# Kernel tuning notes

Measured on AMD Instinct MI355X. Metric: run time of the kernel, lower is better.

## Reference

```python
import jax, jax.numpy as jnp
import numpy as np

ROTARY_DIM = 128
ROTARY_BASE = 10000.0
ATTN_SCALE = 11.313708498984761  # sqrt(d_head=128)
N_HEADS = 16
N_KV = 4


def _apply_rotary(x, rotary_dim, rotary_base):
    # x: [seq, heads, d_head]
    seq_len = x.shape[0]
    dim_pairs = rotary_dim // 2
    freqs = 1.0 / rotary_base ** (jnp.arange(dim_pairs, dtype=jnp.float32) / dim_pairs)
    angles = jnp.outer(jnp.arange(seq_len), freqs)  # [seq, pairs]
    cos = jnp.cos(angles)[:, None, :]
    sin = jnp.sin(angles)[:, None, :]
    x_rot = x[..., :rotary_dim]
    x_pass = x[..., rotary_dim:]
    x1 = x_rot[..., ::2]
    x2 = x_rot[..., 1::2]
    out1 = x1 * cos - x2 * sin
    out2 = x1 * sin + x2 * cos
    rotated = jnp.stack([out1, out2], axis=-1).reshape(x_rot.shape)
    return jnp.concatenate([rotated, x_pass], axis=-1)


def setup_inputs() -> dict:
    key = jax.random.key(0)
    ks = jax.random.split(key, 5)
    seq, d_model, d_head = 4096, 2048, 128
    scale = 1.0 / np.sqrt(d_model)
    return {
        "x": jax.random.normal(ks[0], (seq, d_model), jnp.float32),
        "W_Q": jax.random.normal(ks[1], (N_HEADS, d_model, d_head), jnp.float32) * scale,
        "W_K": jax.random.normal(ks[2], (N_KV, d_model, d_head), jnp.float32) * scale,
        "W_V": jax.random.normal(ks[3], (N_KV, d_model, d_head), jnp.float32) * scale,
        "W_O": jax.random.normal(ks[4], (N_HEADS, d_head, d_model), jnp.float32) * scale,
        "b_Q": jnp.zeros((N_HEADS, d_head), jnp.float32),
        "b_K": jnp.zeros((N_KV, d_head), jnp.float32),
        "b_V": jnp.zeros((N_KV, d_head), jnp.float32),
        "b_O": jnp.zeros((2048,), jnp.float32),
    }


def reference(x, W_Q, W_K, W_V, W_O, b_Q, b_K, b_V, b_O):
    seq_len = x.shape[0]
    q = jnp.einsum('sm,nmh->snh', x, W_Q) + b_Q  # [s, 16, 128]
    k = jnp.einsum('sm,nmh->snh', x, W_K) + b_K  # [s, 4, 128]
    v = jnp.einsum('sm,nmh->snh', x, W_V) + b_V
    q = _apply_rotary(q, ROTARY_DIM, ROTARY_BASE)
    k = _apply_rotary(k, ROTARY_DIM, ROTARY_BASE)
    repeats = N_HEADS // N_KV
    k = jnp.repeat(k, repeats, axis=1)
    v = jnp.repeat(v, repeats, axis=1)
    attn_scores = jnp.einsum('qnh,knh->nqk', q, k) / ATTN_SCALE
    mask = jnp.tril(jnp.ones((seq_len, seq_len), dtype=jnp.bool_))
    attn_scores = jnp.where(mask[None, :, :], attn_scores,
                            jnp.finfo(attn_scores.dtype).min)
    pattern = jax.nn.softmax(attn_scores, axis=-1)
    z = jnp.einsum('nqk,knh->qnh', pattern, v)
    return jnp.einsum('snh,nhm->sm', z, W_O) + b_O
```

## Files before the change

### kernel.cpp

```cpp
#include <hip/hip_runtime.h>
#include <hip/hip_bf16.h>
#include <cstdint>
#include <cstddef>

#define SEQ    4096
#define DM     2048
#define DH     128
#define NH     16
#define NKV    4
#define NC     3072
#define KOFF   2048
#define VOFF   2560
#define Q_SCALE 0.12751730f

using bf16 = __hip_bfloat16;
typedef __bf16 bf16x8 __attribute__((ext_vector_type(8)));
typedef float f32x4 __attribute__((ext_vector_type(4)));
typedef float f32x16 __attribute__((ext_vector_type(16)));

static __device__ inline float bf2f(bf16 x) { return __bfloat162float(x); }
static __device__ inline bf16 f2bf(float x) { return __float2bfloat16(x); }

static __device__ inline void load_lds16(const bf16* g, bf16* l) {
    __builtin_amdgcn_global_load_lds(
        (const __attribute__((address_space(1))) uint32_t*)g,
        (__attribute__((address_space(3))) uint32_t*)l, 16, 0, 0);
}

__global__ void xconv(const float* __restrict__ in, bf16* __restrict__ out) {
    int i = blockIdx.x * 256 + threadIdx.x;
    float4 v = ((const float4*)in)[i];
    bf16 a = f2bf(v.x), b = f2bf(v.y), c = f2bf(v.z), d = f2bf(v.w);
    ushort4 u;
    u.x = *(unsigned short*)&a; u.y = *(unsigned short*)&b;
    u.z = *(unsigned short*)&c; u.w = *(unsigned short*)&d;
    ((ushort4*)out)[i] = u;
}

__global__ void prep_wqkv(const float* __restrict__ WQ, const float* __restrict__ WK,
                          const float* __restrict__ WV, bf16* __restrict__ wt) {
    __shared__ float tl[64][65];
    const int t = threadIdx.x;
    const int m0 = (int)blockIdx.x * 64;
    const int head = (int)blockIdx.y >> 1;
    const int h0 = ((int)blockIdx.y & 1) * 64;
    const float* src = (head < 16) ? WQ + (size_t)head * DM * DH
                     : (head < 20) ? WK + (size_t)(head - 16) * DM * DH
                                   : WV + (size_t)(head - 20) * DM * DH;
    {
        const int r = t >> 2, c = (t & 3) * 16;
        const float* p = src + (size_t)(m0 + r) * DH + h0 + c;
        #pragma unroll
        for (int kk = 0; kk < 4; ++kk) {
            float4 v = *(const float4*)(p + kk * 4);
            tl[r][c + kk * 4 + 0] = v.x; tl[r][c + kk * 4 + 1] = v.y;
            tl[r][c + kk * 4 + 2] = v.z; tl[r][c + kk * 4 + 3] = v.w;
        }
    }
    __syncthreads();
    {
        const int hh = t >> 2, ms = (t & 3) * 16;
        const int j = head * 128 + h0 + hh;
        bf16 tmp[16];
        #pragma unroll
        for (int i = 0; i < 16; ++i) tmp[i] = f2bf(tl[ms + i][hh]);
        bf16* q = wt + (size_t)j * DM + m0 + ms;
        *(bf16x8*)q       = *(bf16x8*)&tmp[0];
        *(bf16x8*)(q + 8) = *(bf16x8*)&tmp[8];
    }
}

__global__ void prep_wo(const float* __restrict__ WO, bf16* __restrict__ wt) {
    __shared__ float tl[64][65];
    const int t = threadIdx.x;
    const int m0 = (int)blockIdx.x * 64;
    const int j0 = (int)blockIdx.y * 64;
    {
        const int r = t >> 2, c = (t & 3) * 16;
        const float* p = WO + (size_t)(m0 + r) * DM + j0 + c;
        #pragma unroll
        for (int kk = 0; kk < 4; ++kk) {
            float4 v = *(const float4*)(p + kk * 4);
            tl[r][c + kk * 4 + 0] = v.x; tl[r][c + kk * 4 + 1] = v.y;
            tl[r][c + kk * 4 + 2] = v.z; tl[r][c + kk * 4 + 3] = v.w;
        }
    }
    __syncthreads();
    {
        const int hh = t >> 2, ms = (t & 3) * 16;
        bf16 tmp[16];
        #pragma unroll
        for (int i = 0; i < 16; ++i) tmp[i] = f2bf(tl[ms + i][hh]);
        bf16* q = wt + (size_t)(j0 + hh) * DM + m0 + ms;
        *(bf16x8*)q       = *(bf16x8*)&tmp[0];
        *(bf16x8*)(q + 8) = *(bf16x8*)&tmp[8];
    }
}

__global__ void prep_bias(const float* __restrict__ bQ, const float* __restrict__ bK,
                          const float* __restrict__ bV, float* __restrict__ bias) {
    int j = blockIdx.x * 256 + threadIdx.x;
    if (j >= NC) return;
    bias[j] = (j < KOFF) ? bQ[j] : (j < VOFF ? bK[j - KOFF] : bV[j - VOFF]);
}

#define BM 128
#define BN 128
#define BK 64

template <typename OutT>
__global__ __launch_bounds__(256)
void gemm_bt(const bf16* __restrict__ A, const bf16* __restrict__ Bt,
             const float* __restrict__ bias, OutT* __restrict__ C, int N) {
    __shared__ __align__(16) bf16 As[BM * BK];
    __shared__ __align__(16) bf16 Bs[BN * BK];
    const int tid = threadIdx.x;
    const int wave = tid >> 6, lane = tid & 63;
    const int quad = lane >> 4, l15 = lane & 15;
    const int wm = (wave >> 1) * 64, wn = (wave & 1) * 64;
    const int m0 = blockIdx.y * BM, n0 = blockIdx.x * BN;

    f32x4 acc[4][4] = {};

    const bf16* gsrc = (wave < 2)
        ? A  + (size_t)(m0 + (wave & 1) * 64) * DM
        : Bt + (size_t)(n0 + (wave & 1) * 64) * DM;
    bf16* lbase = (wave < 2 ? As : Bs) + (wave & 1) * 64 * BK;
    const int lrow = lane >> 3;
    const int gslot = (lane & 7) ^ lrow;
    const bf16* gp = gsrc + (size_t)lrow * DM + gslot * 8;

    const int rsw = l15 & 7;

    for (int k0 = 0; k0 < DM; k0 += BK) {
        __syncthreads();
        #pragma unroll
        for (int cc = 0; cc < 8; ++cc)
            load_lds16(gp + (size_t)cc * 8 * DM + k0, lbase + cc * 8 * BK);
        __syncthreads();

        #pragma unroll
        for (int ks = 0; ks < 2; ++ks) {
            bf16x8 af[4], bfr[4];
            #pragma unroll
            for (int i = 0; i < 4; ++i)
                af[i] = *(const bf16x8*)&As[(wm + i * 16 + l15) * BK + (((ks * 4 + quad) ^ rsw) * 8)];
            #pragma unroll
            for (int j = 0; j < 4; ++j)
                bfr[j] = *(const bf16x8*)&Bs[(wn + j * 16 + l15) * BK + (((ks * 4 + quad) ^ rsw) * 8)];
            #pragma unroll
            for (int i = 0; i < 4; ++i)
                #pragma unroll
                for (int j = 0; j < 4; ++j)
                    acc[i][j] = __builtin_amdgcn_mfma_f32_16x16x32_bf16(af[i], bfr[j], acc[i][j], 0, 0, 0);
        }
    }

    #pragma unroll
    for (int i = 0; i < 4; ++i) {
        int row = m0 + wm + i * 16 + quad * 4;
        #pragma unroll
        for (int j = 0; j < 4; ++j) {
            int col = n0 + wn + j * 16 + l15;
            float bv = bias[col];
            #pragma unroll
            for (int r = 0; r < 4; ++r) {
                float val = acc[i][j][r] + bv;
                if constexpr (sizeof(OutT) == 2)
                    C[(size_t)(row + r) * N + col] = f2bf(val);
                else
                    C[(size_t)(row + r) * N + col] = val;
            }
        }
    }
}

__global__ void sctab(float2* __restrict__ tab) {
    int idx = blockIdx.x * 256 + threadIdx.x;
    int s = idx >> 6, i = idx & 63;
    float inv_freq = __expf(-(float)i * 0.14391156831212788f);
    float ang = (float)s * inv_freq;
    float2 cs;
    cs.x = cosf(ang);
    cs.y = sinf(ang);
    tab[idx] = cs;
}

__global__ void rotary(bf16* __restrict__ qkv, const float2* __restrict__ tab) {
    int idx = blockIdx.x * 256 + threadIdx.x;
    const int QP = SEQ * (NH * DH / 2);
    int s, col, i; float scale;
    if (idx < QP) {
        s = idx >> 10; int p = idx & 1023;
        col = ((p >> 6) * DH) + 2 * (p & 63);
        i = p & 63;
        scale = Q_SCALE;
    } else {
        idx -= QP;
        if (idx >= SEQ * (NKV * DH / 2)) return;
        s = idx >> 8; int p = idx & 255;
        col = KOFF + ((p >> 6) * DH) + 2 * (p & 63);
        i = p & 63;
        scale = 1.0f;
    }
    float2 cs = tab[(s << 6) + i];
    float c = cs.x, sn = cs.y;
    uint32_t u = *(const uint32_t*)(qkv + (size_t)s * NC + col);
    float x1 = __uint_as_float((u & 0xffffu) << 16);
    float x2 = __uint_as_float(u & 0xffff0000u);
    float o1 = (x1 * c - x2 * sn) * scale;
    float o2 = (x1 * sn + x2 * c) * scale;
    bf16 h1 = f2bf(o1), h2 = f2bf(o2);
    uint32_t out = ((uint32_t)(*(unsigned short*)&h2) << 16) | (uint32_t)(*(unsigned short*)&h1);
    *(uint32_t*)(qkv + (size_t)s * NC + col) = out;
}

__global__ void vtrans(const bf16* __restrict__ qkv, bf16* __restrict__ vt) {
    __shared__ bf16 tl[64][72];
    const int t = threadIdx.x;
    const int s0 = (int)(blockIdx.x >> 3) * 64;
    const int c0 = (int)(blockIdx.x & 7) * 64;
    {
        int r = t >> 2, cc = (t & 3) * 16;
        const bf16* p = qkv + (size_t)(s0 + r) * NC + VOFF + c0 + cc;
        *(bf16x8*)&tl[r][cc]     = *(const bf16x8*)p;
        *(bf16x8*)&tl[r][cc + 8] = *(const bf16x8*)(p + 8);
    }
    __syncthreads();
    {
        int dd = t >> 2, sc = (t & 3) * 16;
        int col = c0 + dd;
        bf16 tmp[16];
        #pragma unroll
        for (int j = 0; j < 16; ++j) tmp[j] = tl[sc + j][dd];
        bf16* q = vt + (size_t)col * SEQ + s0 + sc;
        *(bf16x8*)q       = *(bf16x8*)&tmp[0];
        *(bf16x8*)(q + 8) = *(bf16x8*)&tmp[8];
    }
}

__global__ __launch_bounds__(256, 3)
void flash(const bf16* __restrict__ qkv, const bf16* __restrict__ vt,
           bf16* __restrict__ z) {
    __shared__ char smem[33280];
    bf16*  Ks  = (bf16*)smem;
    bf16*  Vs  = (bf16*)(smem + 16384);
    float* lml = (float*)(smem + 32768);
    float* ob  = (float*)smem;

    const int tid = threadIdx.x;
    const int wave = tid >> 6, lane = tid & 63;
    const int l31 = lane & 31, lh = lane >> 5;
    const int ch = wave >> 1;
    const int kh = wave & 1;
    const int bx = blockIdx.x;
    const int qt = 127 - (bx >> 3);
    const int g = (bx >> 1) & 3;
    const int hp = bx & 1;
    const int r_base = qt * 32 + ch * 16;
    const int ktmax = qt >> 1;
    const int rsw = l31 & 7;

    const bf16* kp[4];
    const bf16* vp[4];
    #pragma unroll
    for (int i = 0; i < 4; ++i) {
        const int q = wave * 4 + i;
        const int krow = q * 4 + (lane >> 4);
        kp[i] = qkv + KOFF + g * DH + (size_t)krow * NC + (((lane & 15) ^ (krow & 7)) * 8);
        const int vdd = q * 8 + (lane >> 3);
        vp[i] = vt + (size_t)(g * DH + vdd) * SEQ + (((lane & 7) ^ (vdd & 7)) * 8);
    }

    bf16x8 qf[8];
    {
        const int qrow = r_base + (l31 & 15);
        const int head = g * 4 + hp * 2 + (l31 >> 4);
        const bf16* qp = qkv + (size_t)qrow * NC + head * DH + lh * 8;
        #pragma unroll
        for (int s = 0; s < 8; ++s)
            qf[s] = *(const bf16x8*)(qp + s * 16);
    }

    f32x16 o_acc[4] = {};
    float lsum = 0.0f;

    for (int kt = 0; kt <= ktmax; ++kt) {
        __syncthreads();
        #pragma unroll
        for (int i = 0; i < 4; ++i)
            load_lds16(kp[i], Ks + (wave * 4 + i) * 512);
        #pragma unroll
        for (int i = 0; i < 4; ++i)
            load_lds16(vp[i], Vs + (wave * 4 + i) * 512);
        __syncthreads();
        #pragma unroll
        for (int i = 0; i < 4; ++i) { kp[i] += (size_t)64 * NC; vp[i] += 64; }

        const int key_min = kt * 64 + kh * 32;
        if (key_min <= r_base + 15) {
            f32x16 sacc = {};
            __builtin_amdgcn_s_setprio(1);
            #pragma unroll
            for (int s = 0; s < 8; ++s) {
                bf16x8 kb = *(const bf16x8*)&Ks[(kh * 32 + l31) * 128 + (((lh + 2 * s) ^ rsw) * 8)];
                sacc = __builtin_amdgcn_mfma_f32_32x32x16_bf16(kb, qf[s], sacc, 0, 0, 0);
            }
            __builtin_amdgcn_s_setprio(0);

            const bool needmask = (key_min + 31 > r_base);
            const int qrow = r_base + (l31 & 15);
            float e[16];
            if (needmask) {
                #pragma unroll
                for (int rg = 0; rg < 16; ++rg) {
                    const int keyg = key_min + (rg & 3) + 8 * (rg >> 2) + 4 * lh;
                    float sv = sacc[rg];
                    if (keyg > qrow) sv = -INFINITY;
                    e[rg] = exp2f(sv);
                }
            } else {
                #pragma unroll
                for (int rg = 0; rg < 16; ++rg)
                    e[rg] = exp2f(sacc[rg]);
            }
            {
                float t0 = (e[0] + e[1]) + (e[2] + e[3]);
                float t1 = (e[4] + e[5]) + (e[6] + e[7]);
                float t2 = (e[8] + e[9]) + (e[10] + e[11]);
                float t3 = (e[12] + e[13]) + (e[14] + e[15]);
                lsum += (t0 + t1) + (t2 + t3);
            }

            bf16x8 pa[2];
            #pragma unroll
            for (int s2 = 0; s2 < 2; ++s2) {
                uint32_t wA0, wA1, wB0, wB1;
                asm("v_cvt_pk_bf16_f32 %0, %1, %2" : "=v"(wA0) : "v"(e[8*s2+0]), "v"(e[8*s2+1]));
                asm("v_cvt_pk_bf16_f32 %0, %1, %2" : "=v"(wA1) : "v"(e[8*s2+2]), "v"(e[8*s2+3]));
                asm("v_cvt_pk_bf16_f32 %0, %1, %2" : "=v"(wB0) : "v"(e[8*s2+4]), "v"(e[8*s2+5]));
                asm("v_cvt_pk_bf16_f32 %0, %1, %2" : "=v"(wB1) : "v"(e[8*s2+6]), "v"(e[8*s2+7]));
                asm volatile("v_permlane32_swap_b32 %0, %1" : "+v"(wA0), "+v"(wB0));
                asm volatile("v_permlane32_swap_b32 %0, %1" : "+v"(wA1), "+v"(wB1));
                union { uint32_t u[4]; bf16x8 v; } cvt;
                cvt.u[0] = wA0; cvt.u[1] = wA1; cvt.u[2] = wB0; cvt.u[3] = wB1;
                pa[s2] = cvt.v;
            }

            __builtin_amdgcn_s_setprio(1);
            #pragma unroll
            for (int nt = 0; nt < 4; ++nt) {
                #pragma unroll
                for (int s2 = 0; s2 < 2; ++s2) {
                    bf16x8 vb = *(const bf16x8*)&Vs[(nt * 32 + l31) * 64 + (((kh * 4 + lh + 2 * s2) ^ rsw) * 8)];
                    o_acc[nt] = __builtin_amdgcn_mfma_f32_32x32x16_bf16(pa[s2], vb, o_acc[nt], 0, 0, 0);
                }
            }
            __builtin_amdgcn_s_setprio(0);
        }
    }

    float la = lsum, lb = lsum;
    asm volatile("v_permlane32_swap_b32 %0, %1" : "+v"(la), "+v"(lb));
    const float l_tot = la + lb;

    __syncthreads();
    if (lh == 0) lml[wave * 32 + l31] = l_tot;
    if (kh == 1) {
        #pragma unroll
        for (int nt = 0; nt < 4; ++nt)
            #pragma unroll
            for (int rg = 0; rg < 16; ++rg) {
                const int m = (rg & 3) + 8 * (rg >> 2) + 4 * lh;
                ob[(ch * 32 + m) * 128 + nt * 32 + l31] = o_acc[nt][rg];
            }
    }
    __syncthreads();
    if (kh == 0) {
        float invl[16];
        #pragma unroll
        for (int rg = 0; rg < 16; ++rg) {
            const int m = (rg & 3) + 8 * (rg >> 2) + 4 * lh;
            invl[rg] = 1.0f / (lml[wave * 32 + m] + lml[(wave + 1) * 32 + m]);
        }
        #pragma unroll
        for (int nt = 0; nt < 4; ++nt)
            #pragma unroll
            for (int rg = 0; rg < 16; ++rg) {
                const int m = (rg & 3) + 8 * (rg >> 2) + 4 * lh;
                float oo = o_acc[nt][rg] + ob[(ch * 32 + m) * 128 + nt * 32 + l31];
                const int row = r_base + (m & 15);
                const int col = (g * 4 + hp * 2 + (m >> 4)) * DH + nt * 32 + l31;
                z[(size_t)row * DM + col] = f2bf(oo * invl[rg]);
            }
    }
}

extern "C" void kernel_launch(void* const* d_in, const int* in_sizes, int n_in,
                              void* d_out, int out_size, void* d_ws, size_t ws_size,
                              hipStream_t stream) {
    const float* x  = (const float*)d_in[0];
    const float* WQ = (const float*)d_in[1];
    const float* WK = (const float*)d_in[2];
    const float* WV = (const float*)d_in[3];
    const float* WO = (const float*)d_in[4];
    const float* bQ = (const float*)d_in[5];
    const float* bK = (const float*)d_in[6];
    const float* bV = (const float*)d_in[7];
    const float* bO = (const float*)d_in[8];
    float* out = (float*)d_out;

    char* ws = (char*)d_ws;
    bf16*  wt_cat = (bf16*)(ws);
    bf16*  wt_o   = (bf16*)(ws + 12582912);
    float* bias_c = (float*)(ws + 20971520);
    bf16*  qkv    = (bf16*)(ws + 20987904);
    bf16*  vt     = (bf16*)(ws + 46153728);
    bf16*  z      = (bf16*)(ws + 50348032);
    bf16*  xb     = (bf16*)(ws + 67125248);
    float2* sct   = (float2*)xb;

    xconv    <<<8192, 256, 0, stream>>>(x, xb);
    prep_wqkv<<<dim3(32, 48), 256, 0, stream>>>(WQ, WK, WV, wt_cat);
    prep_wo  <<<dim3(32, 32), 256, 0, stream>>>(WO, wt_o);
    prep_bias<<<12, 256, 0, stream>>>(bQ, bK, bV, bias_c);
    gemm_bt<bf16> <<<dim3(24, 32), 256, 0, stream>>>(xb, wt_cat, bias_c, qkv, NC);
    sctab    <<<1024, 256, 0, stream>>>(sct);
    rotary   <<<20480, 256, 0, stream>>>(qkv, sct);
    vtrans   <<<512, 256, 0, stream>>>(qkv, vt);
    flash    <<<1024, 256, 0, stream>>>(qkv, vt, z);
    gemm_bt<float><<<dim3(16, 32), 256, 0, stream>>>(z, wt_o, bO, out, DM);
}
```

Measured before the change: 354.7 us.

## Fuse rotary into QKV GEMM epilogue and double-buffer flash K/V tiles

Removes the separate rotary kernel by applying rotation and Q scaling in the QKV GEMM epilogue, using a lane shuffle to fetch the paired value. The sin/cos table moves into the vt buffer so it is not overwritten by xb. The flash kernel now double-buffers K/V tiles in 64KB of shared memory, prefetching the next tile while computing the current one, and drops the occupancy hint of 3 blocks. It also splits the QK accumulation into two independent chains and reorders the PV loop. The larger shared memory footprint reduces occupancy.

```diff
diff --git a/kernel.cpp b/kernel.cpp
--- a/kernel.cpp
+++ b/kernel.cpp
@@ -104,77 +104,6 @@
     bias[j] = (j < KOFF) ? bQ[j] : (j < VOFF ? bK[j - KOFF] : bV[j - VOFF]);
 }
 
-#define BM 128
-#define BN 128
-#define BK 64
-
-template <typename OutT>
-__global__ __launch_bounds__(256)
-void gemm_bt(const bf16* __restrict__ A, const bf16* __restrict__ Bt,
-             const float* __restrict__ bias, OutT* __restrict__ C, int N) {
-    __shared__ __align__(16) bf16 As[BM * BK];
-    __shared__ __align__(16) bf16 Bs[BN * BK];
-    const int tid = threadIdx.x;
-    const int wave = tid >> 6, lane = tid & 63;
-    const int quad = lane >> 4, l15 = lane & 15;
-    const int wm = (wave >> 1) * 64, wn = (wave & 1) * 64;
-    const int m0 = blockIdx.y * BM, n0 = blockIdx.x * BN;
-
-    f32x4 acc[4][4] = {};
-
-    const bf16* gsrc = (wave < 2)
-        ? A  + (size_t)(m0 + (wave & 1) * 64) * DM
-        : Bt + (size_t)(n0 + (wave & 1) * 64) * DM;
-    bf16* lbase = (wave < 2 ? As : Bs) + (wave & 1) * 64 * BK;
-    const int lrow = lane >> 3;
-    const int gslot = (lane & 7) ^ lrow;
-    const bf16* gp = gsrc + (size_t)lrow * DM + gslot * 8;
-
-    const int rsw = l15 & 7;
-
-    for (int k0 = 0; k0 < DM; k0 += BK) {
-        __syncthreads();
-        #pragma unroll
-        for (int cc = 0; cc < 8; ++cc)
-            load_lds16(gp + (size_t)cc * 8 * DM + k0, lbase + cc * 8 * BK);
-        __syncthreads();
-
-        #pragma unroll
-        for (int ks = 0; ks < 2; ++ks) {
-            bf16x8 af[4], bfr[4];
-            #pragma unroll
-            for (int i = 0; i < 4; ++i)
-                af[i] = *(const bf16x8*)&As[(wm + i * 16 + l15) * BK + (((ks * 4 + quad) ^ rsw) * 8)];
-            #pragma unroll
-            for (int j = 0; j < 4; ++j)
-                bfr[j] = *(const bf16x8*)&Bs[(wn + j * 16 + l15) * BK + (((ks * 4 + quad) ^ rsw) * 8)];
-            #pragma unroll
-            for (int i = 0; i < 4; ++i)
-                #pragma unroll
-                for (int j = 0; j < 4; ++j)
-                    acc[i][j] = __builtin_amdgcn_mfma_f32_16x16x32_bf16(af[i], bfr[j], acc[i][j], 0, 0, 0);
-        }
-    }
-
-    #pragma unroll
-    for (int i = 0; i < 4; ++i) {
-        int row = m0 + wm + i * 16 + quad * 4;
-        #pragma unroll
-        for (int j = 0; j < 4; ++j) {
-            int col = n0 + wn + j * 16 + l15;
-            float bv = bias[col];
-            #pragma unroll
-            for (int r = 0; r < 4; ++r) {
-                float val = acc[i][j][r] + bv;
-                if constexpr (sizeof(OutT) == 2)
-                    C[(size_t)(row + r) * N + col] = f2bf(val);
-                else
-                    C[(size_t)(row + r) * N + col] = val;
-            }
-        }
-    }
-}
-
 __global__ void sctab(float2* __restrict__ tab) {
     int idx = blockIdx.x * 256 + threadIdx.x;
     int s = idx >> 6, i = idx & 63;
@@ -186,33 +115,92 @@
     tab[idx] = cs;
 }
 
-__global__ void rotary(bf16* __restrict__ qkv, const float2* __restrict__ tab) {
-    int idx = blockIdx.x * 256 + threadIdx.x;
-    const int QP = SEQ * (NH * DH / 2);
-    int s, col, i; float scale;
-    if (idx < QP) {
-        s = idx >> 10; int p = idx & 1023;
-        col = ((p >> 6) * DH) + 2 * (p & 63);
-        i = p & 63;
-        scale = Q_SCALE;
-    } else {
-        idx -= QP;
-        if (idx >= SEQ * (NKV * DH / 2)) return;
-        s = idx >> 8; int p = idx & 255;
-        col = KOFF + ((p >> 6) * DH) + 2 * (p & 63);
-        i = p & 63;
-        scale = 1.0f;
-    }
-    float2 cs = tab[(s << 6) + i];
-    float c = cs.x, sn = cs.y;
-    uint32_t u = *(const uint32_t*)(qkv + (size_t)s * NC + col);
-    float x1 = __uint_as_float((u & 0xffffu) << 16);
-    float x2 = __uint_as_float(u & 0xffff0000u);
-    float o1 = (x1 * c - x2 * sn) * scale;
-    float o2 = (x1 * sn + x2 * c) * scale;
-    bf16 h1 = f2bf(o1), h2 = f2bf(o2);
-    uint32_t out = ((uint32_t)(*(unsigned short*)&h2) << 16) | (uint32_t)(*(unsigned short*)&h1);
-    *(uint32_t*)(qkv + (size_t)s * NC + col) = out;
+#define BM 128
+#define BN 128
+#define BK 64
+
+template <typename OutT, int ROT>
+__global__ __launch_bounds__(256)
+void gemm_bt(const bf16* __restrict__ A, const bf16* __restrict__ Bt,
+             const float* __restrict__ bias, OutT* __restrict__ C, int N,
+             const float2* __restrict__ tab) {
+    __shared__ __align__(16) bf16 As[BM * BK];
+    __shared__ __align__(16) bf16 Bs[BN * BK];
+    const int tid = threadIdx.x;
+    const int wave = tid >> 6, lane = tid & 63;
+    const int quad = lane >> 4, l15 = lane & 15;
+    const int wm = (wave >> 1) * 64, wn = (wave & 1) * 64;
+    const int m0 = blockIdx.y * BM, n0 = blockIdx.x * BN;
+
+    f32x4 acc[4][4] = {};
+
+    const bf16* gsrc = (wave < 2)
+        ? A  + (size_t)(m0 + (wave & 1) * 64) * DM
+        : Bt + (size_t)(n0 + (wave & 1) * 64) * DM;
+    bf16* lbase = (wave < 2 ? As : Bs) + (wave & 1) * 64 * BK;
+    const int lrow = lane >> 3;
+    const int gslot = (lane & 7) ^ lrow;
+    const bf16* gp = gsrc + (size_t)lrow * DM + gslot * 8;
+
+    const int rsw = l15 & 7;
+
+    for (int k0 = 0; k0 < DM; k0 += BK) {
+        __syncthreads();
+        #pragma unroll
+        for (int cc = 0; cc < 8; ++cc)
+            load_lds16(gp + (size_t)cc * 8 * DM + k0, lbase + cc * 8 * BK);
+        __syncthreads();
+
+        #pragma unroll
+        for (int ks = 0; ks < 2; ++ks) {
+            bf16x8 af[4], bfr[4];
+            #pragma unroll
+            for (int i = 0; i < 4; ++i)
+                af[i] = *(const bf16x8*)&As[(wm + i * 16 + l15) * BK + (((ks * 4 + quad) ^ rsw) * 8)];
+            #pragma unroll
+            for (int j = 0; j < 4; ++j)
+                bfr[j] = *(const bf16x8*)&Bs[(wn + j * 16 + l15) * BK + (((ks * 4 + quad) ^ rsw) * 8)];
+            #pragma unroll
+            for (int i = 0; i < 4; ++i)
+                #pragma unroll
+                for (int j = 0; j < 4; ++j)
+                    acc[i][j] = __builtin_amdgcn_mfma_f32_16x16x32_bf16(af[i], bfr[j], acc[i][j], 0, 0, 0);
+        }
+    }
+
+    const bool doRot = ROT && (n0 < VOFF);
+    const float scl = (n0 < KOFF) ? Q_SCALE : 1.0f;
+
+    #pragma unroll
+    for (int i = 0; i < 4; ++i) {
+        int row = m0 + wm + i * 16 + quad * 4;
+        #pragma unroll
+        for (int j = 0; j < 4; ++j) {
+            int col = n0 + wn + j * 16 + l15;
+            float bv = bias[col];
+            if (ROT && doRot) {
+                const int ii = (col >> 1) & 63;
+                const bool odd = col & 1;
+                #pragma unroll
+                for (int r = 0; r < 4; ++r) {
+                    float v = acc[i][j][r] + bv;
+                    float pv = __shfl_xor(v, 1);
+                    float2 cs = tab[((row + r) << 6) + ii];
+                    float o = odd ? (pv * cs.y + v * cs.x) : (v * cs.x - pv * cs.y);
+                    C[(size_t)(row + r) * N + col] = (OutT)f2bf(o * scl);
+                }
+            } else {
+                #pragma unroll
+                for (int r = 0; r < 4; ++r) {
+                    float val = acc[i][j][r] + bv;
+                    if constexpr (sizeof(OutT) == 2)
+                        C[(size_t)(row + r) * N + col] = f2bf(val);
+                    else
+                        C[(size_t)(row + r) * N + col] = val;
+                }
+            }
+        }
+    }
 }
 
 __global__ void vtrans(const bf16* __restrict__ qkv, bf16* __restrict__ vt) {
@@ -239,14 +227,12 @@
     }
 }
 
-__global__ __launch_bounds__(256, 3)
+__global__ __launch_bounds__(256)
 void flash(const bf16* __restrict__ qkv, const bf16* __restrict__ vt,
            bf16* __restrict__ z) {
-    __shared__ char smem[33280];
-    bf16*  Ks  = (bf16*)smem;
-    bf16*  Vs  = (bf16*)(smem + 16384);
+    __shared__ __align__(16) char smem[65536];
+    float* ob  = (float*)smem;
     float* lml = (float*)(smem + 32768);
-    float* ob  = (float*)smem;
 
     const int tid = threadIdx.x;
     const int wave = tid >> 6, lane = tid & 63;
@@ -272,6 +258,17 @@
         vp[i] = vt + (size_t)(g * DH + vdd) * SEQ + (((lane & 7) ^ (vdd & 7)) * 8);
     }
 
+    {
+        bf16* Ksb = (bf16*)smem;
+        bf16* Vsb = (bf16*)(smem + 16384);
+        #pragma unroll
+        for (int i = 0; i < 4; ++i) load_lds16(kp[i], Ksb + (wave * 4 + i) * 512);
+        #pragma unroll
+        for (int i = 0; i < 4; ++i) load_lds16(vp[i], Vsb + (wave * 4 + i) * 512);
+        #pragma unroll
+        for (int i = 0; i < 4; ++i) { kp[i] += (size_t)64 * NC; vp[i] += 64; }
+    }
+
     bf16x8 qf[8];
     {
         const int qrow = r_base + (l31 & 15);
@@ -284,29 +281,37 @@
 
     f32x16 o_acc[4] = {};
     float lsum = 0.0f;
+    int cur = 0;
 
     for (int kt = 0; kt <= ktmax; ++kt) {
         __syncthreads();
-        #pragma unroll
-        for (int i = 0; i < 4; ++i)
-            load_lds16(kp[i], Ks + (wave * 4 + i) * 512);
-        #pragma unroll
-        for (int i = 0; i < 4; ++i)
-            load_lds16(vp[i], Vs + (wave * 4 + i) * 512);
-        __syncthreads();
-        #pragma unroll
-        for (int i = 0; i < 4; ++i) { kp[i] += (size_t)64 * NC; vp[i] += 64; }
+        if (kt < ktmax) {
+            bf16* Ksb = (bf16*)(smem + (cur ^ 1) * 32768);
+            bf16* Vsb = (bf16*)(smem + (cur ^ 1) * 32768 + 16384);
+            #pragma unroll
+            for (int i = 0; i < 4; ++i) load_lds16(kp[i], Ksb + (wave * 4 + i) * 512);
+            #pragma unroll
+            for (int i = 0; i < 4; ++i) load_lds16(vp[i], Vsb + (wave * 4 + i) * 512);
+            #pragma unroll
+            for (int i = 0; i < 4; ++i) { kp[i] += (size_t)64 * NC; vp[i] += 64; }
+        }
+        const bf16* Ks = (const bf16*)(smem + cur * 32768);
+        const bf16* Vs = (const bf16*)(smem + cur * 32768 + 16384);
+        cur ^= 1;
 
         const int key_min = kt * 64 + kh * 32;
         if (key_min <= r_base + 15) {
-            f32x16 sacc = {};
+            f32x16 sa = {}, sb = {};
             __builtin_amdgcn_s_setprio(1);
             #pragma unroll
-            for (int s = 0; s < 8; ++s) {
-                bf16x8 kb = *(const bf16x8*)&Ks[(kh * 32 + l31) * 128 + (((lh + 2 * s) ^ rsw) * 8)];
-                sacc = __builtin_amdgcn_mfma_f32_32x32x16_bf16(kb, qf[s], sacc, 0, 0, 0);
+            for (int s = 0; s < 4; ++s) {
+                bf16x8 kb0 = *(const bf16x8*)&Ks[(kh * 32 + l31) * 128 + (((lh + 4 * s) ^ rsw) * 8)];
+                sa = __builtin_amdgcn_mfma_f32_32x32x16_bf16(kb0, qf[2 * s], sa, 0, 0, 0);
+                bf16x8 kb1 = *(const bf16x8*)&Ks[(kh * 32 + l31) * 128 + (((lh + 4 * s + 2) ^ rsw) * 8)];
+                sb = __builtin_amdgcn_mfma_f32_32x32x16_bf16(kb1, qf[2 * s + 1], sb, 0, 0, 0);
             }
             __builtin_amdgcn_s_setprio(0);
+            f32x16 sacc = sa + sb;
 
             const bool needmask = (key_min + 31 > r_base);
             const int qrow = r_base + (l31 & 15);
@@ -349,9 +354,9 @@
 
             __builtin_amdgcn_s_setprio(1);
             #pragma unroll
-            for (int nt = 0; nt < 4; ++nt) {
-                #pragma unroll
-                for (int s2 = 0; s2 < 2; ++s2) {
+            for (int s2 = 0; s2 < 2; ++s2) {
+                #pragma unroll
+                for (int nt = 0; nt < 4; ++nt) {
                     bf16x8 vb = *(const bf16x8*)&Vs[(nt * 32 + l31) * 64 + (((kh * 4 + lh + 2 * s2) ^ rsw) * 8)];
                     o_acc[nt] = __builtin_amdgcn_mfma_f32_32x32x16_bf16(pa[s2], vb, o_acc[nt], 0, 0, 0);
                 }
@@ -418,16 +423,15 @@
     bf16*  vt     = (bf16*)(ws + 46153728);
     bf16*  z      = (bf16*)(ws + 50348032);
     bf16*  xb     = (bf16*)(ws + 67125248);
-    float2* sct   = (float2*)xb;
+    float2* sct   = (float2*)vt;
 
     xconv    <<<8192, 256, 0, stream>>>(x, xb);
     prep_wqkv<<<dim3(32, 48), 256, 0, stream>>>(WQ, WK, WV, wt_cat);
     prep_wo  <<<dim3(32, 32), 256, 0, stream>>>(WO, wt_o);
     prep_bias<<<12, 256, 0, stream>>>(bQ, bK, bV, bias_c);
-    gemm_bt<bf16> <<<dim3(24, 32), 256, 0, stream>>>(xb, wt_cat, bias_c, qkv, NC);
     sctab    <<<1024, 256, 0, stream>>>(sct);
-    rotary   <<<20480, 256, 0, stream>>>(qkv, sct);
+    gemm_bt<bf16, 1> <<<dim3(24, 32), 256, 0, stream>>>(xb, wt_cat, bias_c, qkv, NC, sct);
     vtrans   <<<512, 256, 0, stream>>>(qkv, vt);
     flash    <<<1024, 256, 0, stream>>>(qkv, vt, z);
-    gemm_bt<float><<<dim3(16, 32), 256, 0, stream>>>(z, wt_o, bO, out, DM);
-}
+    gemm_bt<float, 0><<<dim3(16, 32), 256, 0, stream>>>(z, wt_o, bO, out, DM, nullptr);
+}
```

After: 376.5 us. 1.06x slower.
